# Kernel optimization log

Measured on AMD Instinct MI355X. Metric: run time of the kernel, lower is better.

Reference implementation:

```python
import jax, jax.numpy as jnp
import numpy as np

C = 256
CQK = C // 8  # query/key projection dim (in_dim // 8)
B, H, W = 4, 64, 64


def setup_inputs() -> dict:
    key = jax.random.key(0)
    ks = jax.random.split(key, 7)
    scale = 0.05
    x = jax.random.normal(ks[0], (B, C, H, W), dtype=jnp.float32)
    Wq = jax.random.normal(ks[1], (CQK, C), dtype=jnp.float32) * scale
    bq = jax.random.normal(ks[2], (CQK,), dtype=jnp.float32) * scale
    Wk = jax.random.normal(ks[3], (CQK, C), dtype=jnp.float32) * scale
    bk = jax.random.normal(ks[4], (CQK,), dtype=jnp.float32) * scale
    Wv = jax.random.normal(ks[5], (C, C), dtype=jnp.float32) * scale
    bv = jax.random.normal(ks[6], (C,), dtype=jnp.float32) * scale
    return {"x": x, "Wq": Wq, "bq": bq, "Wk": Wk, "bk": bk, "Wv": Wv, "bv": bv}


def reference(x, Wq, bq, Wk, bk, Wv, bv):
    b, c, h, w = x.shape
    n = h * w
    xf = x.reshape(b, c, n)  # [B, C, N]
    # 1x1 convs == per-pixel linear maps over channels
    q = jnp.einsum('dc,bcn->bnd', Wq, xf) + bq[None, None, :]   # [B, N, C/8]
    k = jnp.einsum('dc,bcn->bdn', Wk, xf) + bk[None, :, None]   # [B, C/8, N]
    v = jnp.einsum('dc,bcn->bdn', Wv, xf) + bv[None, :, None]   # [B, C, N]
    energy = jnp.einsum('bnd,bdm->bnm', q, k)                    # [B, N, N]
    attention = jax.nn.softmax(energy, axis=-1)                  # softmax over keys
    # out = V @ attention^T  (torch: bmm(proj_value, attention.permute(0,2,1)))
    out = jnp.einsum('bdm,bnm->bdn', v, attention)               # [B, C, N]
    return out.reshape(b, c, h, w) + x
```

## Files before the change

### kernel.cpp

```cpp
#include <hip/hip_runtime.h>
#include <math.h>

#define BATCH 4
#define CH    256
#define NPIX  4096
#define DQK   32

typedef short          s16;
typedef unsigned int   uint_t;
typedef __attribute__((ext_vector_type(8))) short short8;
typedef __attribute__((ext_vector_type(4))) float floatx4;

__device__ __forceinline__ s16 f2bf(float f) {
  union { float f; uint_t u; } v; v.f = f;
  return (s16)((v.u + 0x8000u) >> 16);
}
__device__ __forceinline__ uint_t pk2(float a, float b) {
  union { float f; uint_t u; } x, y; x.f = a; y.f = b;
  return (((y.u + 0x8000u) >> 16) << 16) | ((x.u + 0x8000u) >> 16);
}

__global__ __launch_bounds__(256) void prepack(
    const float* __restrict__ Wq, const float* __restrict__ bq,
    const float* __restrict__ Wk, const float* __restrict__ bk,
    const float* __restrict__ Wv, const float* __restrict__ bv,
    s16* __restrict__ Wbf, float* __restrict__ Bsw)
{
  const int gid = blockIdx.x * 256 + threadIdx.x;
  const int e0  = gid * 4;
  const int row = e0 >> 8, col = e0 & 255;
  const float* src = (row < 32) ? Wq + (size_t)row * 256
                   : (row < 64) ? Wk + (size_t)(row - 32) * 256
                                : Wv + (size_t)(row - 64) * 256;
  float4 f = *(const float4*)(src + col);
  uint2 o; o.x = pk2(f.x, f.y); o.y = pk2(f.z, f.w);
  *(uint2*)(Wbf + e0) = o;
  if (gid < 320)
    Bsw[gid] = (gid < 32) ? bq[gid] : (gid < 64) ? bk[gid - 32] : bv[gid - 64];
}

__global__ __launch_bounds__(256, 2) void proj_mfma(
    const float* __restrict__ x, const s16* __restrict__ Wbf,
    const float* __restrict__ Bsw,
    s16* __restrict__ Qw, s16* __restrict__ Kw, s16* __restrict__ Vw)
{
  const int b  = blockIdx.x >> 7;
  const int n0 = (blockIdx.x & 127) << 5;
  const int t  = threadIdx.x;

  __shared__ s16 Xs[32][264];
  __shared__ s16 Os[256][40];

  const float* xb = x + (size_t)b * CH * NPIX + n0;
  #pragma unroll
  for (int i = 0; i < 2; ++i) {
    int task = i * 256 + t;
    int ncg  = task & 7;
    int kcg  = task >> 3;
    const float* src = xb + (size_t)(kcg * 4) * NPIX + ncg * 4;
    float rows[4][4];
    *(float4*)&rows[0][0] = *(const float4*)(src);
    *(float4*)&rows[1][0] = *(const float4*)(src + NPIX);
    *(float4*)&rows[2][0] = *(const float4*)(src + 2 * NPIX);
    *(float4*)&rows[3][0] = *(const float4*)(src + 3 * NPIX);
    #pragma unroll
    for (int c = 0; c < 4; ++c) {
      uint2 pk;
      pk.x = pk2(rows[0][c], rows[1][c]);
      pk.y = pk2(rows[2][c], rows[3][c]);
      *(uint2*)&Xs[ncg * 4 + c][kcg * 4] = pk;
    }
  }
  __syncthreads();

  const int w    = t >> 6;
  const int l15  = t & 15;
  const int quad = (t & 63) >> 4;

  floatx4 acc[5][2];
  #pragma unroll
  for (int si = 0; si < 5; ++si)
    #pragma unroll
    for (int nt = 0; nt < 2; ++nt) acc[si][nt] = (floatx4){0.f, 0.f, 0.f, 0.f};

  short8 afc[5], afn[5];
  #pragma unroll
  for (int si = 0; si < 5; ++si) {
    const int s = w + si * 4;
    afc[si] = *(const short8*)(Wbf + (size_t)(s * 16 + l15) * 256 + quad * 8);
  }
  for (int kc = 0; kc < 8; ++kc) {
    const int k0  = kc * 32;
    const int kn0 = (kc < 7) ? k0 + 32 : 0;
    #pragma unroll
    for (int si = 0; si < 5; ++si) {
      const int s = w + si * 4;
      afn[si] = *(const short8*)(Wbf + (size_t)(s * 16 + l15) * 256 + kn0 + quad * 8);
    }
    short8 bf[2];
    #pragma unroll
    for (int nt = 0; nt < 2; ++nt)
      bf[nt] = *(const short8*)&Xs[l15 + 16 * nt][k0 + quad * 8];
    #pragma unroll
    for (int si = 0; si < 5; ++si)
      #pragma unroll
      for (int nt = 0; nt < 2; ++nt)
        acc[si][nt] = __builtin_amdgcn_mfma_f32_16x16x32_bf16(afc[si], bf[nt], acc[si][nt], 0, 0, 0);
    #pragma unroll
    for (int si = 0; si < 5; ++si) afc[si] = afn[si];
  }

  #pragma unroll
  for (int si = 0; si < 5; ++si) {
    const int s = w + si * 4;
    float4 bb = *(const float4*)(Bsw + 16 * s + quad * 4);
    #pragma unroll
    for (int nt = 0; nt < 2; ++nt) {
      const int px  = 16 * nt + l15;
      float v0 = acc[si][nt][0] + bb.x;
      float v1 = acc[si][nt][1] + bb.y;
      float v2 = acc[si][nt][2] + bb.z;
      float v3 = acc[si][nt][3] + bb.w;
      if (s < 4) {
        s16* dst = (s < 2) ? Qw : Kw;
        int d0 = (s & 1) * 16 + quad * 4;
        uint2 pq; pq.x = pk2(v0, v1); pq.y = pk2(v2, v3);
        *(uint2*)(dst + ((size_t)b * NPIX + n0 + px) * DQK + d0) = pq;
      } else {
        const int c0 = (s - 4) * 16 + quad * 4;
        Os[c0 + 0][px] = f2bf(v0);
        Os[c0 + 1][px] = f2bf(v1);
        Os[c0 + 2][px] = f2bf(v2);
        Os[c0 + 3][px] = f2bf(v3);
      }
    }
  }
  __syncthreads();
  #pragma unroll
  for (int rep = 0; rep < 4; ++rep) {
    const int task = rep * 256 + t;
    const int ch   = task >> 2;
    const int seg  = task & 3;
    *(uint4*)(Vw + ((size_t)b * CH + ch) * NPIX + n0 + seg * 8) =
        *(const uint4*)&Os[ch][seg * 8];
  }
}

__global__ __launch_bounds__(512, 4) void attn_mfma(
    const s16* __restrict__ Qw, const s16* __restrict__ Kw,
    const s16* __restrict__ Vw, const float* __restrict__ x,
    float* __restrict__ out)
{
  const int bi = blockIdx.x;
  const int b  = (bi & 7) >> 1;
  const int h  = bi & 1;
  const int qt = bi >> 3;
  const int n0 = qt * 64;
  const int t  = threadIdx.x;
  const int w    = t >> 6;
  const int l15  = t & 15;
  const int quad = (t & 63) >> 4;
  const int cb   = h * 128 + 16 * w;

  __shared__ s16  Pt[2][64][136];
  __shared__ float Lsum[64][8];

  const s16* qbase = Qw + ((size_t)b * NPIX + n0) * DQK;
  short8 qb[4];
  #pragma unroll
  for (int tq = 0; tq < 4; ++tq)
    qb[tq] = *(const short8*)(qbase + (size_t)(16 * tq + l15) * DQK + quad * 8);

  floatx4 o[4];
  #pragma unroll
  for (int tq = 0; tq < 4; ++tq) o[tq] = (floatx4){0.f, 0.f, 0.f, 0.f};
  float l_part[4] = {0.f, 0.f, 0.f, 0.f};

  const s16* kbase = Kw + (size_t)b * NPIX * DQK;
  const s16* vbase = Vw + (size_t)b * CH * NPIX;

  short8 ka_c, ka_n, va[4];
  ka_c = *(const short8*)(kbase + (size_t)(16 * w + l15) * DQK + quad * 8);
  #pragma unroll
  for (int j = 0; j < 4; ++j)
    va[j] = *(const short8*)(vbase + (size_t)(cb + l15) * NPIX + 32 * j + quad * 8);

  int buf = 0;
  for (int kt = 0; kt < 32; ++kt) {
    const int m0  = kt * 128;
    const int mn0 = (kt < 31) ? m0 + 128 : 0;

    floatx4 sacc[4];
    #pragma unroll
    for (int tq = 0; tq < 4; ++tq)
      sacc[tq] = __builtin_amdgcn_mfma_f32_16x16x32_bf16(
                   ka_c, qb[tq], (floatx4){0.f, 0.f, 0.f, 0.f}, 0, 0, 0);

    ka_n = *(const short8*)(kbase + (size_t)(mn0 + 16 * w + l15) * DQK + quad * 8);

    #pragma unroll
    for (int tq = 0; tq < 4; ++tq) {
      float p0 = __expf(fminf(sacc[tq][0], 60.f));
      float p1 = __expf(fminf(sacc[tq][1], 60.f));
      float p2 = __expf(fminf(sacc[tq][2], 60.f));
      float p3 = __expf(fminf(sacc[tq][3], 60.f));
      l_part[tq] += (p0 + p1) + (p2 + p3);
      uint2 pk; pk.x = pk2(p0, p1); pk.y = pk2(p2, p3);
      *(uint2*)&Pt[buf][16 * tq + l15][16 * w + quad * 4] = pk;
    }
    __syncthreads();

    #pragma unroll
    for (int j = 0; j < 4; ++j) {
      short8 pb[4];
      #pragma unroll
      for (int tq = 0; tq < 4; ++tq)
        pb[tq] = *(const short8*)&Pt[buf][16 * tq + l15][32 * j + quad * 8];
      #pragma unroll
      for (int tq = 0; tq < 4; ++tq)
        o[tq] = __builtin_amdgcn_mfma_f32_16x16x32_bf16(va[j], pb[tq], o[tq], 0, 0, 0);
    }
    #pragma unroll
    for (int j = 0; j < 4; ++j)
      va[j] = *(const short8*)(vbase + (size_t)(cb + l15) * NPIX + mn0 + 32 * j + quad * 8);

    ka_c = ka_n;
    buf ^= 1;
  }

  #pragma unroll
  for (int tq = 0; tq < 4; ++tq) {
    l_part[tq] += __shfl_xor(l_part[tq], 16);
    l_part[tq] += __shfl_xor(l_part[tq], 32);
  }
  if (quad == 0) {
    #pragma unroll
    for (int tq = 0; tq < 4; ++tq) Lsum[16 * tq + l15][w] = l_part[tq];
  }
  __syncthreads();

  float inv[4];
  #pragma unroll
  for (int tq = 0; tq < 4; ++tq) {
    float4 s0 = *(const float4*)&Lsum[16 * tq + l15][0];
    float4 s1 = *(const float4*)&Lsum[16 * tq + l15][4];
    inv[tq] = 1.f / (((s0.x + s0.y) + (s0.z + s0.w)) + ((s1.x + s1.y) + (s1.z + s1.w)));
  }

  #pragma unroll
  for (int tq = 0; tq < 4; ++tq) {
    const int npx = n0 + 16 * tq + l15;
    #pragma unroll
    for (int r = 0; r < 4; ++r) {
      const int c = cb + quad * 4 + r;
      const size_t off = ((size_t)b * CH + c) * NPIX + npx;
      out[off] = fmaf(o[tq][r], inv[tq], x[off]);
    }
  }
}

extern "C" void kernel_launch(void* const* d_in, const int* in_sizes, int n_in,
                              void* d_out, int out_size, void* d_ws, size_t ws_size,
                              hipStream_t stream) {
  (void)in_sizes; (void)n_in; (void)out_size; (void)ws_size;
  const float* x  = (const float*)d_in[0];
  const float* Wq = (const float*)d_in[1];
  const float* bq = (const float*)d_in[2];
  const float* Wk = (const float*)d_in[3];
  const float* bk = (const float*)d_in[4];
  const float* Wv = (const float*)d_in[5];
  const float* bv = (const float*)d_in[6];
  float* out = (float*)d_out;

  unsigned char* ws = (unsigned char*)d_ws;
  s16*   Qw  = (s16*)ws;
  s16*   Kw  = (s16*)(ws + (size_t)1 * 1024 * 1024);
  s16*   Vw  = (s16*)(ws + (size_t)2 * 1024 * 1024);
  s16*   Wbf = (s16*)(ws + (size_t)10 * 1024 * 1024);
  float* Bsw = (float*)(ws + (size_t)10 * 1024 * 1024 + 256 * 1024);

  hipLaunchKernelGGL(prepack, dim3(80), dim3(256), 0, stream,
                     Wq, bq, Wk, bk, Wv, bv, Wbf, Bsw);
  hipLaunchKernelGGL(proj_mfma, dim3(512), dim3(256), 0, stream,
                     x, Wbf, Bsw, Qw, Kw, Vw);
  hipLaunchKernelGGL(attn_mfma, dim3(512), dim3(512), 0, stream,
                     Qw, Kw, Vw, x, out);
}
```

Baseline: 166.2 us.

## Cover all channels per block with 32x32 MFMA and swizzled P tile

The attention kernel now has each block cover all 256 value channels for its 64 queries, using 32x32x16 bf16 MFMAs, instead of splitting channels across two blocks. This halves the grid and avoids computing QK^T and exp twice per query tile. It also replaces the padded P shared-memory layout with an XOR swizzle to avoid bank conflicts. The trade-off is more registers (16-wide accumulators, 8 V fragments), so occupancy drops to two blocks per CU, and there are fewer blocks than before.

```diff
diff --git a/kernel.cpp b/kernel.cpp
--- a/kernel.cpp
+++ b/kernel.cpp
@@ -10,6 +10,7 @@
 typedef unsigned int   uint_t;
 typedef __attribute__((ext_vector_type(8))) short short8;
 typedef __attribute__((ext_vector_type(4))) float floatx4;
+typedef __attribute__((ext_vector_type(16))) float floatx16;
 
 __device__ __forceinline__ s16 f2bf(float f) {
   union { float f; uint_t u; } v; v.f = f;
@@ -146,23 +147,25 @@
   }
 }
 
-__global__ __launch_bounds__(512, 4) void attn_mfma(
+__global__ __launch_bounds__(512, 2) void attn_mfma(
     const s16* __restrict__ Qw, const s16* __restrict__ Kw,
     const s16* __restrict__ Vw, const float* __restrict__ x,
     float* __restrict__ out)
 {
   const int bi = blockIdx.x;
-  const int b  = (bi & 7) >> 1;
-  const int h  = bi & 1;
-  const int qt = bi >> 3;
+  const int b  = bi & 3;
+  const int qt = bi >> 2;
   const int n0 = qt * 64;
   const int t  = threadIdx.x;
   const int w    = t >> 6;
   const int l15  = t & 15;
   const int quad = (t & 63) >> 4;
-  const int cb   = h * 128 + 16 * w;
-
-  __shared__ s16  Pt[2][64][136];
+  const int l31  = t & 31;
+  const int lh   = (t & 63) >> 5;
+  const int l7   = t & 7;
+  const int cb   = 32 * w;
+
+  __shared__ s16  Pt[2][64][128];
   __shared__ float Lsum[64][8];
 
   const s16* qbase = Qw + ((size_t)b * NPIX + n0) * DQK;
@@ -171,19 +174,19 @@
   for (int tq = 0; tq < 4; ++tq)
     qb[tq] = *(const short8*)(qbase + (size_t)(16 * tq + l15) * DQK + quad * 8);
 
-  floatx4 o[4];
-  #pragma unroll
-  for (int tq = 0; tq < 4; ++tq) o[tq] = (floatx4){0.f, 0.f, 0.f, 0.f};
+  floatx16 o[2];
+  #pragma unroll
+  for (int i = 0; i < 16; ++i) { o[0][i] = 0.f; o[1][i] = 0.f; }
   float l_part[4] = {0.f, 0.f, 0.f, 0.f};
 
   const s16* kbase = Kw + (size_t)b * NPIX * DQK;
-  const s16* vbase = Vw + (size_t)b * CH * NPIX;
-
-  short8 ka_c, ka_n, va[4];
+  const s16* vbase = Vw + ((size_t)b * CH + cb) * NPIX;
+
+  short8 ka_c, ka_n, va[8];
   ka_c = *(const short8*)(kbase + (size_t)(16 * w + l15) * DQK + quad * 8);
   #pragma unroll
-  for (int j = 0; j < 4; ++j)
-    va[j] = *(const short8*)(vbase + (size_t)(cb + l15) * NPIX + 32 * j + quad * 8);
+  for (int ks = 0; ks < 8; ++ks)
+    va[ks] = *(const short8*)(vbase + (size_t)l31 * NPIX + 16 * ks + 8 * lh);
 
   int buf = 0;
   for (int kt = 0; kt < 32; ++kt) {
@@ -198,6 +201,7 @@
 
     ka_n = *(const short8*)(kbase + (size_t)(mn0 + 16 * w + l15) * DQK + quad * 8);
 
+    const int wslot = (((2 * w + (quad >> 1)) ^ l7) << 3) + (quad & 1) * 4;
     #pragma unroll
     for (int tq = 0; tq < 4; ++tq) {
       float p0 = __expf(fminf(sacc[tq][0], 60.f));
@@ -206,23 +210,21 @@
       float p3 = __expf(fminf(sacc[tq][3], 60.f));
       l_part[tq] += (p0 + p1) + (p2 + p3);
       uint2 pk; pk.x = pk2(p0, p1); pk.y = pk2(p2, p3);
-      *(uint2*)&Pt[buf][16 * tq + l15][16 * w + quad * 4] = pk;
+      *(uint2*)&Pt[buf][16 * tq + l15][wslot] = pk;
     }
     __syncthreads();
 
     #pragma unroll
-    for (int j = 0; j < 4; ++j) {
-      short8 pb[4];
-      #pragma unroll
-      for (int tq = 0; tq < 4; ++tq)
-        pb[tq] = *(const short8*)&Pt[buf][16 * tq + l15][32 * j + quad * 8];
-      #pragma unroll
-      for (int tq = 0; tq < 4; ++tq)
-        o[tq] = __builtin_amdgcn_mfma_f32_16x16x32_bf16(va[j], pb[tq], o[tq], 0, 0, 0);
-    }
-    #pragma unroll
-    for (int j = 0; j < 4; ++j)
-      va[j] = *(const short8*)(vbase + (size_t)(cb + l15) * NPIX + mn0 + 32 * j + quad * 8);
+    for (int ks = 0; ks < 8; ++ks) {
+      const int rslot = ((2 * ks + lh) ^ l7) << 3;
+      short8 pb0 = *(const short8*)&Pt[buf][l31     ][rslot];
+      short8 pb1 = *(const short8*)&Pt[buf][32 + l31][rslot];
+      o[0] = __builtin_amdgcn_mfma_f32_32x32x16_bf16(va[ks], pb0, o[0], 0, 0, 0);
+      o[1] = __builtin_amdgcn_mfma_f32_32x32x16_bf16(va[ks], pb1, o[1], 0, 0, 0);
+    }
+    #pragma unroll
+    for (int ks = 0; ks < 8; ++ks)
+      va[ks] = *(const short8*)(vbase + (size_t)l31 * NPIX + mn0 + 16 * ks + 8 * lh);
 
     ka_c = ka_n;
     buf ^= 1;
@@ -239,22 +241,19 @@
   }
   __syncthreads();
 
-  float inv[4];
-  #pragma unroll
-  for (int tq = 0; tq < 4; ++tq) {
-    float4 s0 = *(const float4*)&Lsum[16 * tq + l15][0];
-    float4 s1 = *(const float4*)&Lsum[16 * tq + l15][4];
-    inv[tq] = 1.f / (((s0.x + s0.y) + (s0.z + s0.w)) + ((s1.x + s1.y) + (s1.z + s1.w)));
-  }
-
-  #pragma unroll
-  for (int tq = 0; tq < 4; ++tq) {
-    const int npx = n0 + 16 * tq + l15;
-    #pragma unroll
-    for (int r = 0; r < 4; ++r) {
-      const int c = cb + quad * 4 + r;
+  #pragma unroll
+  for (int half = 0; half < 2; ++half) {
+    const int q = half * 32 + l31;
+    float4 s0 = *(const float4*)&Lsum[q][0];
+    float4 s1 = *(const float4*)&Lsum[q][4];
+    float invq = 1.f / (((s0.x + s0.y) + (s0.z + s0.w)) +
+                        ((s1.x + s1.y) + (s1.z + s1.w)));
+    const int npx = n0 + q;
+    #pragma unroll
+    for (int r = 0; r < 16; ++r) {
+      const int c = cb + (r & 3) + 8 * (r >> 2) + 4 * lh;
       const size_t off = ((size_t)b * CH + c) * NPIX + npx;
-      out[off] = fmaf(o[tq][r], inv[tq], x[off]);
+      out[off] = fmaf(o[half][r], invq, x[off]);
     }
   }
 }
@@ -283,6 +282,6 @@
                      Wq, bq, Wk, bk, Wv, bv, Wbf, Bsw);
   hipLaunchKernelGGL(proj_mfma, dim3(512), dim3(256), 0, stream,
                      x, Wbf, Bsw, Qw, Kw, Vw);
-  hipLaunchKernelGGL(attn_mfma, dim3(512), dim3(512), 0, stream,
+  hipLaunchKernelGGL(attn_mfma, dim3(256), dim3(512), 0, stream,
                      Qw, Kw, Vw, x, out);
 }
```

Measured after the change: 158.1 us. 4.9% less time.
